# Performance work log

Hardware: AMD Instinct MI355X
Metric: run time of the kernel (lower is better)

## Reference

```python
import jax, jax.numpy as jnp
import numpy as np

N_NODES = 50000
N_EDGES = 1600000
IN_DIM = 128
HID = 64
N_GRAPHS = 256


def gcn_conv(x, row, col, W, b, n_nodes):
    """PyG GCNConv: symmetric gcn_norm with self-loops, linear-then-aggregate."""
    h = x @ W  # [N, out]
    loop = jnp.arange(n_nodes, dtype=row.dtype)
    r = jnp.concatenate([row, loop])  # sources (messages from x[r])
    c = jnp.concatenate([col, loop])  # targets (aggregate at c)
    ew = jnp.ones(r.shape[0], dtype=x.dtype)
    deg = jax.ops.segment_sum(ew, c, num_segments=n_nodes)
    dinv = jnp.where(deg > 0, jax.lax.rsqrt(deg), 0.0).astype(x.dtype)
    norm = dinv[r] * dinv[c]  # [E+N]
    out = jax.ops.segment_sum(norm[:, None] * h[r], c, num_segments=n_nodes)
    return out + b


def global_mean_pool(x, batch, n_graphs):
    sums = jax.ops.segment_sum(x, batch, num_segments=n_graphs)
    cnt = jax.ops.segment_sum(jnp.ones(x.shape[0], x.dtype), batch, num_segments=n_graphs)
    return sums / jnp.clip(cnt, 1.0)[:, None]


def setup_inputs() -> dict:
    key = jax.random.key(0)
    ks = jax.random.split(key, 12)
    x = jax.random.normal(ks[0], (N_NODES, IN_DIM), dtype=jnp.float32)
    edge_index = jax.random.randint(ks[1], (2, N_EDGES), 0, N_NODES, dtype=jnp.int64)
    batch = jnp.sort(jax.random.randint(ks[2], (N_NODES,), 0, N_GRAPHS, dtype=jnp.int64))
    def glorot(k, shp):
        lim = float(np.sqrt(6.0 / (shp[0] + shp[1])))
        return jax.random.uniform(k, shp, jnp.float32, -lim, lim)
    return {
        "x": x,
        "edge_index": edge_index,
        "batch": batch,
        "W1": glorot(ks[3], (IN_DIM, HID)), "b1": jnp.zeros((HID,), jnp.float32),
        "W2": glorot(ks[4], (HID, HID)), "b2": jnp.zeros((HID,), jnp.float32),
        "W3": glorot(ks[5], (HID, HID)), "b3": jnp.zeros((HID,), jnp.float32),
        "Wl1": glorot(ks[6], (HID, 16)), "bl1": jnp.zeros((16,), jnp.float32),
        "Wl2": glorot(ks[7], (16, 1)), "bl2": jnp.zeros((1,), jnp.float32),
    }


def reference(x, edge_index, batch, W1, b1, W2, b2, W3, b3, Wl1, bl1, Wl2, bl2):
    n = x.shape[0]
    row, col = edge_index[0], edge_index[1]
    h = jax.nn.relu(gcn_conv(x, row, col, W1, b1, n))
    h = jax.nn.relu(gcn_conv(h, row, col, W2, b2, n))
    h = jax.nn.relu(gcn_conv(h, row, col, W3, b3, n))
    g = global_mean_pool(h, batch, N_GRAPHS)  # [G, 64]
    out = (g @ Wl1 + bl1) @ Wl2 + bl2  # [G, 1]
    return out
```

## Files before the change

### kernel.cpp

```cpp
#include <hip/hip_runtime.h>

#define HID 64
#define B1 256
#define NBMAX 200
#define CAP 10368

__device__ __forceinline__ ushort f2bf(float f) {
  unsigned u = __float_as_uint(f);
  unsigned r = (u + 0x7fffu + ((u >> 16) & 1u)) >> 16;
  return (ushort)r;
}
__device__ __forceinline__ float bf2f(ushort v) {
  return __uint_as_float(((unsigned)v) << 16);
}


__global__ __launch_bounds__(256) void bucket_hist(const int* __restrict__ col, int E, int epb,
                                                   int nb, int* __restrict__ blockcnt) {
  __shared__ int cnt[NBMAX];
  int b = blockIdx.x, t = threadIdx.x;
  for (int i = t; i < nb; i += 256) cnt[i] = 0;
  __syncthreads();
  int lo = b * epb, hi = min(lo + epb, E);
  for (int e = lo + t; e < hi; e += 256) atomicAdd(&cnt[col[e] >> 8], 1);
  __syncthreads();
  for (int i = t; i < nb; i += 256) blockcnt[i * B1 + b] = cnt[i];
}

__global__ __launch_bounds__(256) void scan_blockcnt(int* __restrict__ blockcnt,
                                                     int* __restrict__ buckettot) {
  __shared__ int s[256];
  int k = blockIdx.x, t = threadIdx.x;
  int v = blockcnt[k * B1 + t];
  s[t] = v;
  __syncthreads();
  for (int d = 1; d < 256; d <<= 1) {
    int u = (t >= d) ? s[t - d] : 0;
    __syncthreads();
    s[t] += u;
    __syncthreads();
  }
  blockcnt[k * B1 + t] = s[t] - v;
  if (t == 255) buckettot[k] = s[255];
}

__global__ __launch_bounds__(256) void scan_buckettot(const int* __restrict__ buckettot,
                                                      int* __restrict__ bucketbase,
                                                      int* __restrict__ csr_off, int n, int E,
                                                      int nb) {
  __shared__ int s[256];
  int t = threadIdx.x;
  int v = (t < nb) ? buckettot[t] : 0;
  s[t] = v;
  __syncthreads();
  for (int d = 1; d < 256; d <<= 1) {
    int u = (t >= d) ? s[t - d] : 0;
    __syncthreads();
    s[t] += u;
    __syncthreads();
  }
  if (t <= nb) bucketbase[t] = (t == 0) ? 0 : s[t - 1];
  if (t == 0) csr_off[n] = E;
}

__global__ __launch_bounds__(256) void bin_edges(const int* __restrict__ row,
                                                 const int* __restrict__ col, int E, int epb,
                                                 int nb, const int* __restrict__ blockcnt,
                                                 const int* __restrict__ bucketbase,
                                                 unsigned* __restrict__ binned) {
  __shared__ int woff[NBMAX];
  int b = blockIdx.x, t = threadIdx.x;
  for (int i = t; i < nb; i += 256) woff[i] = blockcnt[i * B1 + b] + bucketbase[i];
  __syncthreads();
  int lo = b * epb, hi = min(lo + epb, E);
  for (int e = lo + t; e < hi; e += 256) {
    int c = col[e];
    int r = row[e];
    int pos = atomicAdd(&woff[c >> 8], 1);
    binned[pos] = ((unsigned)r << 8) | (unsigned)(c & 255);
  }
}

__global__ __launch_bounds__(256) void bucket_csr(const unsigned* __restrict__ binned,
                                                  const int* __restrict__ bucketbase,
                                                  int* __restrict__ csr_off,
                                                  int* __restrict__ csr_src,
                                                  float* __restrict__ dinv, int n) {
  __shared__ int lcnt[256];
  __shared__ int lofs[256];
  __shared__ int lsrc[CAP];
  int k = blockIdx.x, t = threadIdx.x;
  int base = bucketbase[k], end = bucketbase[k + 1];
  int s = end - base;
  lcnt[t] = 0;
  __syncthreads();
  for (int i = t; i < s; i += 256) {
    unsigned p = binned[base + i];
    atomicAdd(&lcnt[p & 255u], 1);
  }
  __syncthreads();
  int v = lcnt[t];
  lofs[t] = v;
  __syncthreads();
  for (int d = 1; d < 256; d <<= 1) {
    int u = (t >= d) ? lofs[t - d] : 0;
    __syncthreads();
    lofs[t] += u;
    __syncthreads();
  }
  int excl = lofs[t] - v;
  int node = (k << 8) + t;
  if (node < n) {
    csr_off[node] = base + excl;
    dinv[node] = rsqrtf((float)(v + 1));
  }
  lcnt[t] = excl;
  __syncthreads();
  for (int i = t; i < s; i += 256) {
    unsigned p = binned[base + i];
    int pos = atomicAdd(&lcnt[p & 255u], 1);
    if (pos < CAP) lsrc[pos] = (int)(p >> 8);
  }
  __syncthreads();
  for (int i = t; i < s; i += 256) csr_src[base + i] = (i < CAP) ? lsrc[i] : 0;
}


template <int K>
__global__ __launch_bounds__(256) void gemm_scale_kernel(
    const float* __restrict__ X, const float* __restrict__ W,
    const float* __restrict__ dinv, ushort* __restrict__ out, int n) {
  __shared__ float xs[64][K + 1];
  __shared__ float wsm[K][HID];
  int tid = threadIdx.x;
  int rb = blockIdx.x * 64;

  const float4* W4 = (const float4*)W;
  float4* ws4 = (float4*)&wsm[0][0];
  for (int i = tid; i < K * 16; i += 256) ws4[i] = W4[i];

  for (int i = tid; i < K * 16; i += 256) {
    int r = i / (K / 4);
    int cc = i - r * (K / 4);
    int row = rb + r;
    float4 v = make_float4(0.f, 0.f, 0.f, 0.f);
    if (row < n) v = ((const float4*)X)[row * (K / 4) + cc];
    xs[r][cc * 4 + 0] = v.x;
    xs[r][cc * 4 + 1] = v.y;
    xs[r][cc * 4 + 2] = v.z;
    xs[r][cc * 4 + 3] = v.w;
  }
  __syncthreads();

  int tx = tid & 15;
  int ty = tid >> 4;
  float acc[4][4] = {};
#pragma unroll 8
  for (int k = 0; k < K; ++k) {
    float4 w4 = *(const float4*)&wsm[k][tx * 4];
    float x0 = xs[ty * 4 + 0][k];
    float x1 = xs[ty * 4 + 1][k];
    float x2 = xs[ty * 4 + 2][k];
    float x3 = xs[ty * 4 + 3][k];
    acc[0][0] += x0 * w4.x; acc[0][1] += x0 * w4.y; acc[0][2] += x0 * w4.z; acc[0][3] += x0 * w4.w;
    acc[1][0] += x1 * w4.x; acc[1][1] += x1 * w4.y; acc[1][2] += x1 * w4.z; acc[1][3] += x1 * w4.w;
    acc[2][0] += x2 * w4.x; acc[2][1] += x2 * w4.y; acc[2][2] += x2 * w4.z; acc[2][3] += x2 * w4.w;
    acc[3][0] += x3 * w4.x; acc[3][1] += x3 * w4.y; acc[3][2] += x3 * w4.z; acc[3][3] += x3 * w4.w;
  }

#pragma unroll
  for (int j = 0; j < 4; ++j) {
    int row = rb + ty * 4 + j;
    if (row < n) {
      float sc = dinv[row];
      ushort4 o;
      o.x = f2bf(acc[j][0] * sc);
      o.y = f2bf(acc[j][1] * sc);
      o.z = f2bf(acc[j][2] * sc);
      o.w = f2bf(acc[j][3] * sc);
      ((ushort4*)out)[row * 16 + tx] = o;
    }
  }
}


__global__ __launch_bounds__(256) void agg_kernel(
    const ushort* __restrict__ hs, const int* __restrict__ csr_off,
    const int* __restrict__ csr_src, const float* __restrict__ dinv,
    const float* __restrict__ bias, float* __restrict__ out, int n) {
  int wid = (blockIdx.x * 256 + threadIdx.x) >> 6;
  int lane = threadIdx.x & 63;
  if (wid >= n) return;
  float acc = bf2f(hs[wid * 64 + lane]);
  int j = csr_off[wid];
  int e = csr_off[wid + 1];
  for (; j + 4 <= e; j += 4) {
    int r0 = csr_src[j + 0];
    int r1 = csr_src[j + 1];
    int r2 = csr_src[j + 2];
    int r3 = csr_src[j + 3];
    ushort a0 = hs[r0 * 64 + lane];
    ushort a1 = hs[r1 * 64 + lane];
    ushort a2 = hs[r2 * 64 + lane];
    ushort a3 = hs[r3 * 64 + lane];
    acc += bf2f(a0);
    acc += bf2f(a1);
    acc += bf2f(a2);
    acc += bf2f(a3);
  }
  for (; j < e; ++j) acc += bf2f(hs[csr_src[j] * 64 + lane]);
  float v = dinv[wid] * acc + bias[lane];
  out[wid * 64 + lane] = fmaxf(v, 0.f);
}


__global__ __launch_bounds__(256) void pool_mlp_kernel(
    const float* __restrict__ a, const int* __restrict__ batch, int n,
    const float* __restrict__ Wl1, const float* __restrict__ bl1,
    const float* __restrict__ Wl2, const float* __restrict__ bl2,
    float* __restrict__ out) {
  int g = blockIdx.x;
  int t = threadIdx.x;
  int lane = t & 63;
  int w = t >> 6;

  int lo = 0, hi = n;
  while (lo < hi) {
    int m = (lo + hi) >> 1;
    if (batch[m] < g) lo = m + 1; else hi = m;
  }
  int start = lo;
  lo = start; hi = n;
  while (lo < hi) {
    int m = (lo + hi) >> 1;
    if (batch[m] < g + 1) lo = m + 1; else hi = m;
  }
  int end = lo;

  float s = 0.f;
  for (int i = start + w; i < end; i += 4) s += a[i * 64 + lane];

  __shared__ float ps[4][64];
  __shared__ float gv[64];
  __shared__ float hv[16];
  ps[w][lane] = s;
  __syncthreads();
  if (w == 0) {
    float tot = ps[0][lane] + ps[1][lane] + ps[2][lane] + ps[3][lane];
    gv[lane] = tot / (float)max(end - start, 1);
  }
  __syncthreads();
  if (t < 16) {
    float h = bl1[t];
    for (int k = 0; k < 64; ++k) h += gv[k] * Wl1[k * 16 + t];
    hv[t] = h;
  }
  __syncthreads();
  if (t == 0) {
    float o = bl2[0];
    for (int j2 = 0; j2 < 16; ++j2) o += hv[j2] * Wl2[j2];
    out[g] = o;
  }
}


extern "C" void kernel_launch(void* const* d_in, const int* in_sizes, int n_in,
                              void* d_out, int out_size, void* d_ws, size_t ws_size,
                              hipStream_t stream) {
  const float* x = (const float*)d_in[0];
  const int* ei = (const int*)d_in[1];
  const int* batch = (const int*)d_in[2];
  const float* W1 = (const float*)d_in[3];
  const float* b1 = (const float*)d_in[4];
  const float* W2 = (const float*)d_in[5];
  const float* b2 = (const float*)d_in[6];
  const float* W3 = (const float*)d_in[7];
  const float* b3 = (const float*)d_in[8];
  const float* Wl1 = (const float*)d_in[9];
  const float* bl1 = (const float*)d_in[10];
  const float* Wl2 = (const float*)d_in[11];
  const float* bl2 = (const float*)d_in[12];

  int n = in_sizes[0] / 128;
  int E = in_sizes[1] / 2;
  int G = out_size;
  int nb = (n + 255) >> 8;
  int epb = (E + B1 - 1) / B1;

  const int* row = ei;
  const int* col = ei + E;

  char* p = (char*)d_ws;
  int* blockcnt = (int*)p;    p += (size_t)NBMAX * B1 * 4;
  int* buckettot = (int*)p;   p += 256 * 4;
  int* bucketbase = (int*)p;  p += 256 * 4;
  int* csr_off = (int*)p;     p += 50064 * 4;
  float* dinv = (float*)p;    p += 50016 * 4;
  int* csr_src = (int*)p;     p += (size_t)((E + 15) / 16 * 16) * 4;
  ushort* hs = (ushort*)p;    p += (size_t)n * 64 * 2;
  float* abuf = (float*)p;
  unsigned* binned = (unsigned*)hs;

  bucket_hist<<<B1, 256, 0, stream>>>(col, E, epb, nb, blockcnt);
  scan_blockcnt<<<nb, 256, 0, stream>>>(blockcnt, buckettot);
  scan_buckettot<<<1, 256, 0, stream>>>(buckettot, bucketbase, csr_off, n, E, nb);
  bin_edges<<<B1, 256, 0, stream>>>(row, col, E, epb, nb, blockcnt, bucketbase, binned);
  bucket_csr<<<nb, 256, 0, stream>>>(binned, bucketbase, csr_off, csr_src, dinv, n);

  int gblocks = (n + 63) / 64;
  int ablocks = (n * 64 + 255) / 256;

  gemm_scale_kernel<128><<<gblocks, 256, 0, stream>>>(x, W1, dinv, hs, n);
  agg_kernel<<<ablocks, 256, 0, stream>>>(hs, csr_off, csr_src, dinv, b1, abuf, n);
  gemm_scale_kernel<64><<<gblocks, 256, 0, stream>>>(abuf, W2, dinv, hs, n);
  agg_kernel<<<ablocks, 256, 0, stream>>>(hs, csr_off, csr_src, dinv, b2, abuf, n);
  gemm_scale_kernel<64><<<gblocks, 256, 0, stream>>>(abuf, W3, dinv, hs, n);
  agg_kernel<<<ablocks, 256, 0, stream>>>(hs, csr_off, csr_src, dinv, b3, abuf, n);
  pool_mlp_kernel<<<G, 256, 0, stream>>>(abuf, batch, n, Wl1, bl1, Wl2, bl2, (float*)d_out);
}
```

Baseline: 375.8 us.

## Use split-bf16 MFMA for dense GEMMs and pack bf16 pairs in aggregation

After: 348.2 us. 7.3% less time.

```diff
diff --git a/kernel.cpp b/kernel.cpp
--- a/kernel.cpp
+++ b/kernel.cpp
@@ -5,6 +5,9 @@
 #define NBMAX 200
 #define CAP 10368
 
+typedef __attribute__((ext_vector_type(8))) short short8;
+typedef __attribute__((ext_vector_type(4))) float float4v;
+
 __device__ __forceinline__ ushort f2bf(float f) {
   unsigned u = __float_as_uint(f);
   unsigned r = (u + 0x7fffu + ((u >> 16) & 1u)) >> 16;
@@ -12,6 +15,12 @@
 }
 __device__ __forceinline__ float bf2f(ushort v) {
   return __uint_as_float(((unsigned)v) << 16);
+}
+__device__ __forceinline__ float2 unpack2(unsigned u) {
+  float2 r;
+  r.x = __uint_as_float(u << 16);
+  r.y = __uint_as_float(u & 0xffff0000u);
+  return r;
 }
 
 
@@ -126,59 +135,85 @@
 }
 
 
+__global__ __launch_bounds__(256) void prep_w(const float* __restrict__ W1,
+                                              const float* __restrict__ W2,
+                                              const float* __restrict__ W3,
+                                              ushort* __restrict__ Wt1h, ushort* __restrict__ Wt1l,
+                                              ushort* __restrict__ Wt2h, ushort* __restrict__ Wt2l,
+                                              ushort* __restrict__ Wt3h, ushort* __restrict__ Wt3l) {
+  int t = blockIdx.x * 256 + threadIdx.x;
+  if (t < 128 * 64) {
+    int k = t >> 6, nn = t & 63;
+    float w = W1[t];
+    ushort h = f2bf(w);
+    Wt1h[nn * 128 + k] = h;
+    Wt1l[nn * 128 + k] = f2bf(w - bf2f(h));
+  }
+  if (t < 64 * 64) {
+    int k = t >> 6, nn = t & 63;
+    float w2 = W2[t], w3 = W3[t];
+    ushort h2 = f2bf(w2), h3 = f2bf(w3);
+    Wt2h[nn * 64 + k] = h2;
+    Wt2l[nn * 64 + k] = f2bf(w2 - bf2f(h2));
+    Wt3h[nn * 64 + k] = h3;
+    Wt3l[nn * 64 + k] = f2bf(w3 - bf2f(h3));
+  }
+}
+
+
 template <int K>
-__global__ __launch_bounds__(256) void gemm_scale_kernel(
-    const float* __restrict__ X, const float* __restrict__ W,
-    const float* __restrict__ dinv, ushort* __restrict__ out, int n) {
-  __shared__ float xs[64][K + 1];
-  __shared__ float wsm[K][HID];
-  int tid = threadIdx.x;
-  int rb = blockIdx.x * 64;
-
-  const float4* W4 = (const float4*)W;
-  float4* ws4 = (float4*)&wsm[0][0];
-  for (int i = tid; i < K * 16; i += 256) ws4[i] = W4[i];
-
-  for (int i = tid; i < K * 16; i += 256) {
-    int r = i / (K / 4);
-    int cc = i - r * (K / 4);
-    int row = rb + r;
-    float4 v = make_float4(0.f, 0.f, 0.f, 0.f);
-    if (row < n) v = ((const float4*)X)[row * (K / 4) + cc];
-    xs[r][cc * 4 + 0] = v.x;
-    xs[r][cc * 4 + 1] = v.y;
-    xs[r][cc * 4 + 2] = v.z;
-    xs[r][cc * 4 + 3] = v.w;
-  }
-  __syncthreads();
-
-  int tx = tid & 15;
-  int ty = tid >> 4;
-  float acc[4][4] = {};
-#pragma unroll 8
-  for (int k = 0; k < K; ++k) {
-    float4 w4 = *(const float4*)&wsm[k][tx * 4];
-    float x0 = xs[ty * 4 + 0][k];
-    float x1 = xs[ty * 4 + 1][k];
-    float x2 = xs[ty * 4 + 2][k];
-    float x3 = xs[ty * 4 + 3][k];
-    acc[0][0] += x0 * w4.x; acc[0][1] += x0 * w4.y; acc[0][2] += x0 * w4.z; acc[0][3] += x0 * w4.w;
-    acc[1][0] += x1 * w4.x; acc[1][1] += x1 * w4.y; acc[1][2] += x1 * w4.z; acc[1][3] += x1 * w4.w;
-    acc[2][0] += x2 * w4.x; acc[2][1] += x2 * w4.y; acc[2][2] += x2 * w4.z; acc[2][3] += x2 * w4.w;
-    acc[3][0] += x3 * w4.x; acc[3][1] += x3 * w4.y; acc[3][2] += x3 * w4.z; acc[3][3] += x3 * w4.w;
-  }
-
-#pragma unroll
-  for (int j = 0; j < 4; ++j) {
-    int row = rb + ty * 4 + j;
-    if (row < n) {
-      float sc = dinv[row];
-      ushort4 o;
-      o.x = f2bf(acc[j][0] * sc);
-      o.y = f2bf(acc[j][1] * sc);
-      o.z = f2bf(acc[j][2] * sc);
-      o.w = f2bf(acc[j][3] * sc);
-      ((ushort4*)out)[row * 16 + tx] = o;
+__global__ __launch_bounds__(256) void gemm_mfma(const float* __restrict__ A,
+                                                 const ushort* __restrict__ Wh,
+                                                 const ushort* __restrict__ Wl,
+                                                 const float* __restrict__ dinv,
+                                                 ushort* __restrict__ out, int n) {
+  int wave = (blockIdx.x * 256 + threadIdx.x) >> 6;
+  int lane = threadIdx.x & 63;
+  int row0 = wave * 16;
+  if (row0 >= n) return;
+  int m = lane & 15;
+  int quad = lane >> 4;
+  int r = row0 + m;
+  int rc = (r < n) ? r : (n - 1);
+
+  float4v acc[4];
+#pragma unroll
+  for (int t = 0; t < 4; ++t) acc[t] = (float4v){0.f, 0.f, 0.f, 0.f};
+
+#pragma unroll
+  for (int k0 = 0; k0 < K; k0 += 32) {
+    const float4* xp = (const float4*)&A[(size_t)rc * K + k0 + quad * 8];
+    float4 a0 = xp[0];
+    float4 a1 = xp[1];
+    float av[8] = {a0.x, a0.y, a0.z, a0.w, a1.x, a1.y, a1.z, a1.w};
+    short8 ah, al;
+#pragma unroll
+    for (int i = 0; i < 8; ++i) {
+      ushort h = f2bf(av[i]);
+      ah[i] = (short)h;
+      al[i] = (short)f2bf(av[i] - bf2f(h));
+    }
+#pragma unroll
+    for (int t = 0; t < 4; ++t) {
+      size_t wof = (size_t)(t * 16 + m) * K + k0 + quad * 8;
+      short8 bh = *(const short8*)&Wh[wof];
+      short8 bl = *(const short8*)&Wl[wof];
+      acc[t] = __builtin_amdgcn_mfma_f32_16x16x32_bf16(ah, bh, acc[t], 0, 0, 0);
+      acc[t] = __builtin_amdgcn_mfma_f32_16x16x32_bf16(al, bh, acc[t], 0, 0, 0);
+      acc[t] = __builtin_amdgcn_mfma_f32_16x16x32_bf16(ah, bl, acc[t], 0, 0, 0);
+    }
+  }
+
+  float4 dv = ((const float4*)dinv)[(row0 >> 2) + quad];
+  float dvi[4] = {dv.x, dv.y, dv.z, dv.w};
+#pragma unroll
+  for (int i = 0; i < 4; ++i) {
+    int orow = row0 + quad * 4 + i;
+    if (orow < n) {
+#pragma unroll
+      for (int t = 0; t < 4; ++t) {
+        out[(size_t)orow * 64 + t * 16 + m] = f2bf(dvi[i] * acc[t][i]);
+      }
     }
   }
 }
@@ -191,26 +226,48 @@
   int wid = (blockIdx.x * 256 + threadIdx.x) >> 6;
   int lane = threadIdx.x & 63;
   if (wid >= n) return;
-  float acc = bf2f(hs[wid * 64 + lane]);
+  int half = lane >> 5;
+  int fp = lane & 31;
+  const unsigned* hs2 = (const unsigned*)hs;
+
+  float2 acc = make_float2(0.f, 0.f);
+  if (half == 0) {
+    float2 s = unpack2(hs2[(size_t)wid * 32 + fp]);
+    acc.x += s.x; acc.y += s.y;
+  }
+
   int j = csr_off[wid];
   int e = csr_off[wid + 1];
-  for (; j + 4 <= e; j += 4) {
-    int r0 = csr_src[j + 0];
-    int r1 = csr_src[j + 1];
-    int r2 = csr_src[j + 2];
-    int r3 = csr_src[j + 3];
-    ushort a0 = hs[r0 * 64 + lane];
-    ushort a1 = hs[r1 * 64 + lane];
-    ushort a2 = hs[r2 * 64 + lane];
-    ushort a3 = hs[r3 * 64 + lane];
-    acc += bf2f(a0);
-    acc += bf2f(a1);
-    acc += bf2f(a2);
-    acc += bf2f(a3);
-  }
-  for (; j < e; ++j) acc += bf2f(hs[csr_src[j] * 64 + lane]);
-  float v = dinv[wid] * acc + bias[lane];
-  out[wid * 64 + lane] = fmaxf(v, 0.f);
+  int j2 = j + half;
+  for (; j2 + 8 <= e; j2 += 8) {
+    int s0 = csr_src[j2 + 0];
+    int s1 = csr_src[j2 + 2];
+    int s2 = csr_src[j2 + 4];
+    int s3 = csr_src[j2 + 6];
+    unsigned v0 = hs2[(size_t)s0 * 32 + fp];
+    unsigned v1 = hs2[(size_t)s1 * 32 + fp];
+    unsigned v2 = hs2[(size_t)s2 * 32 + fp];
+    unsigned v3 = hs2[(size_t)s3 * 32 + fp];
+    float2 f0 = unpack2(v0), f1 = unpack2(v1), f2 = unpack2(v2), f3 = unpack2(v3);
+    acc.x += f0.x + f1.x + f2.x + f3.x;
+    acc.y += f0.y + f1.y + f2.y + f3.y;
+  }
+  for (; j2 < e; j2 += 2) {
+    float2 f = unpack2(hs2[(size_t)csr_src[j2] * 32 + fp]);
+    acc.x += f.x; acc.y += f.y;
+  }
+
+  acc.x += __shfl_xor(acc.x, 32, 64);
+  acc.y += __shfl_xor(acc.y, 32, 64);
+
+  if (half == 0) {
+    float d = dinv[wid];
+    float2 bi = ((const float2*)bias)[fp];
+    float2 r;
+    r.x = fmaxf(d * acc.x + bi.x, 0.f);
+    r.y = fmaxf(d * acc.y + bi.y, 0.f);
+    ((float2*)out)[(size_t)wid * 32 + fp] = r;
+  }
 }
 
 
@@ -296,6 +353,12 @@
   int* bucketbase = (int*)p;  p += 256 * 4;
   int* csr_off = (int*)p;     p += 50064 * 4;
   float* dinv = (float*)p;    p += 50016 * 4;
+  ushort* Wt1h = (ushort*)p;  p += 128 * 64 * 2;
+  ushort* Wt1l = (ushort*)p;  p += 128 * 64 * 2;
+  ushort* Wt2h = (ushort*)p;  p += 64 * 64 * 2;
+  ushort* Wt2l = (ushort*)p;  p += 64 * 64 * 2;
+  ushort* Wt3h = (ushort*)p;  p += 64 * 64 * 2;
+  ushort* Wt3l = (ushort*)p;  p += 64 * 64 * 2;
   int* csr_src = (int*)p;     p += (size_t)((E + 15) / 16 * 16) * 4;
   ushort* hs = (ushort*)p;    p += (size_t)n * 64 * 2;
   float* abuf = (float*)p;
@@ -305,16 +368,18 @@
   scan_blockcnt<<<nb, 256, 0, stream>>>(blockcnt, buckettot);
   scan_buckettot<<<1, 256, 0, stream>>>(buckettot, bucketbase, csr_off, n, E, nb);
   bin_edges<<<B1, 256, 0, stream>>>(row, col, E, epb, nb, blockcnt, bucketbase, binned);
+  prep_w<<<32, 256, 0, stream>>>(W1, W2, W3, Wt1h, Wt1l, Wt2h, Wt2l, Wt3h, Wt3l);
   bucket_csr<<<nb, 256, 0, stream>>>(binned, bucketbase, csr_off, csr_src, dinv, n);
 
-  int gblocks = (n + 63) / 64;
+  int nwaves = (n + 15) / 16;
+  int gblocks = (nwaves + 3) / 4;
   int ablocks = (n * 64 + 255) / 256;
 
-  gemm_scale_kernel<128><<<gblocks, 256, 0, stream>>>(x, W1, dinv, hs, n);
+  gemm_mfma<128><<<gblocks, 256, 0, stream>>>(x, Wt1h, Wt1l, dinv, hs, n);
   agg_kernel<<<ablocks, 256, 0, stream>>>(hs, csr_off, csr_src, dinv, b1, abuf, n);
-  gemm_scale_kernel<64><<<gblocks, 256, 0, stream>>>(abuf, W2, dinv, hs, n);
+  gemm_mfma<64><<<gblocks, 256, 0, stream>>>(abuf, Wt2h, Wt2l, dinv, hs, n);
   agg_kernel<<<ablocks, 256, 0, stream>>>(hs, csr_off, csr_src, dinv, b2, abuf, n);
-  gemm_scale_kernel<64><<<gblocks, 256, 0, stream>>>(abuf, W3, dinv, hs, n);
+  gemm_mfma<64><<<gblocks, 256, 0, stream>>>(abuf, Wt3h, Wt3l, dinv, hs, n);
   agg_kernel<<<ablocks, 256, 0, stream>>>(hs, csr_off, csr_src, dinv, b3, abuf, n);
   pool_mlp_kernel<<<G, 256, 0, stream>>>(abuf, batch, n, Wl1, bl1, Wl2, bl2, (float*)d_out);
 }
```
